# Performance work log

Hardware: AMD Instinct MI355X
Metric: run time of the kernel (lower is better)

The kernel has to match this reference:

```python
import jax, jax.numpy as jnp
import numpy as np

B, T, C, L = 128, 1024, 128, 128
EPS = 1e-7        # keras.backend.epsilon()
NEG = -1e30       # log-space -inf surrogate


def setup_inputs() -> dict:
    key = jax.random.key(0)
    k1, k2, k3, k4 = jax.random.split(key, 4)
    logits = jax.random.normal(k1, (B, T, C), dtype=jnp.float32)
    y_pred = jax.nn.softmax(logits, axis=-1)                      # ctc_batch_cost expects probs
    y_true = jax.random.randint(k2, (B, L), 0, C - 1)             # blank = C-1 excluded from labels
    input_len = jax.random.randint(k3, (B, 1), T // 2, T + 1)
    label_len = jax.random.randint(k4, (B, 1), L // 2, L + 1)
    return {"y_true": y_true, "y_pred": y_pred, "input_len": input_len, "label_len": label_len}


def _ctc_loss(y_pred, y_true, input_len, label_len):
    # Faithful port of keras ctc_batch_cost: blank index = C-1, merge repeated,
    # log(y_pred + eps), returns per-sample loss with shape [B, 1].
    log_probs = jnp.log(y_pred + EPS)                             # [B,T,C]
    b, t_max, c = log_probs.shape
    blank = c - 1
    l = y_true.shape[1]
    s = 2 * l + 1
    # extended label sequence: blank, l1, blank, l2, ..., blank   [B,S]
    ext = jnp.full((b, s), blank, dtype=y_true.dtype).at[:, 1::2].set(y_true)
    # emission log-prob of each extended symbol at each frame     [B,T,S]
    lp_ext = jnp.take_along_axis(
        log_probs, jnp.broadcast_to(ext[:, None, :], (b, t_max, s)), axis=2)
    # skip transition s-2 -> s allowed iff ext[s] != blank and ext[s] != ext[s-2]
    allow_skip = jnp.concatenate(
        [jnp.zeros((b, 2), bool), (ext[:, 2:] != blank) & (ext[:, 2:] != ext[:, :-2])], axis=1)
    alpha0 = jnp.full((b, s), NEG, dtype=log_probs.dtype).at[:, 0].set(0.0)
    in_len = input_len.reshape(b, 1).astype(jnp.int32)

    def step(alpha, xt):
        lp_t, t = xt                                              # lp_t: [B,S]
        a1 = jnp.pad(alpha[:, :-1], ((0, 0), (1, 0)), constant_values=NEG)
        a2 = jnp.where(allow_skip,
                       jnp.pad(alpha[:, :-2], ((0, 0), (2, 0)), constant_values=NEG), NEG)
        new = lp_t + jnp.logaddexp(jnp.logaddexp(alpha, a1), a2)
        new = jnp.where(t < in_len, new, alpha)                   # freeze past input_len
        return new, None

    alpha, _ = jax.lax.scan(step, alpha0, (jnp.swapaxes(lp_ext, 0, 1), jnp.arange(t_max)))
    lab = label_len.reshape(b, 1).astype(jnp.int32)
    a_last = jnp.take_along_axis(alpha, 2 * lab, axis=1)          # ends at final blank
    a_prev = jnp.take_along_axis(alpha, jnp.maximum(2 * lab - 1, 0), axis=1)  # or final label
    return -jnp.logaddexp(a_last, a_prev)                         # [B,1]


def reference(y_true, y_pred, input_len, label_len):
    return _ctc_loss(y_pred, y_true, input_len, label_len)
```

## Files before the change

kernel.cpp:

```cpp
#include <hip/hip_runtime.h>
#include <cstdint>

#define NB 128
#define NT 1024
#define NC 128
#define NL 128
#define NS 257
#define EPSF 1e-7f
#define LN2F 0.69314718055994530942f
#define NEGL2 -1.442695e30f

typedef float __attribute__((ext_vector_type(2))) v2f;

__device__ __forceinline__ float fexp2(float x){ return __builtin_amdgcn_exp2f(x); }
__device__ __forceinline__ float flog2(float x){ return __builtin_amdgcn_logf(x); }

__device__ __forceinline__ float shup1(float x){
    int r = __builtin_amdgcn_update_dpp(0, __float_as_int(x), 0x138, 0xf, 0xf, true);
    return __int_as_float(r);
}
__device__ __forceinline__ int shup1i(int x){
    return __builtin_amdgcn_update_dpp(0, x, 0x138, 0xf, 0xf, true);
}

__device__ __forceinline__ void dma16(const float* g, float* lds){
    __builtin_amdgcn_global_load_lds((const __attribute__((address_space(1))) void*)g,
                                     (__attribute__((address_space(3))) void*)lds,
                                     16, 0, 0);
}

#define VM_DRAIN() asm volatile("s_waitcnt vmcnt(0)" ::: "memory")

#define AS3U(p) ((unsigned)(size_t)(__attribute__((address_space(3))) void*)(p))

#define WAITLGKM(N) do{ asm volatile("s_waitcnt lgkmcnt(" #N ")" ::: "memory"); \
                        __builtin_amdgcn_sched_barrier(0); }while(0)

#define FILLA(S, O0,O1,O2,O3) do{ \
  asm volatile("ds_read2st64_b32 %0, %1 offset0:" #O0 " offset1:" #O1 : "=v"(S##B2[0]) : "v"(aB)); \
  asm volatile("ds_read2st64_b32 %0, %1 offset0:" #O2 " offset1:" #O3 : "=v"(S##B2[1]) : "v"(aB)); \
  asm volatile("ds_read2st64_b32 %0, %1 offset0:" #O0 " offset1:" #O1 : "=v"(S##A2[0]) : "v"(aA)); \
  asm volatile("ds_read2st64_b32 %0, %1 offset0:" #O2 " offset1:" #O3 : "=v"(S##A2[1]) : "v"(aA)); \
  asm volatile("ds_read2st64_b32 %0, %1 offset0:" #O0 " offset1:" #O1 : "=v"(S##C2[0]) : "v"(aC)); \
  asm volatile("ds_read2st64_b32 %0, %1 offset0:" #O2 " offset1:" #O3 : "=v"(S##C2[1]) : "v"(aC)); \
}while(0)

#define GROUP(S, gg) do{ \
    const v2f pb0 = S##B2[0] + E2, pa0 = S##A2[0] + E2, pc0 = S##C2[0] + E2; \
    const v2f pb1 = S##B2[1] + E2, pa1 = S##A2[1] + E2, pc1 = S##C2[1] + E2; \
    { const bool c_ = !freeze || ((k*32 + (gg)*4 + 0) < Tn); step1(pb0.x, pa0.x, pc0.x, c_); } \
    shm3 = shup1(m3); \
    { const bool c_ = !freeze || ((k*32 + (gg)*4 + 1) < Tn); step1(pb0.y, pa0.y, pc0.y, c_); } \
    shm3 = shup1(m3); \
    { const bool c_ = !freeze || ((k*32 + (gg)*4 + 2) < Tn); step1(pb1.x, pa1.x, pc1.x, c_); } \
    shm3 = shup1(m3); \
    { const bool c_ = !freeze || ((k*32 + (gg)*4 + 3) < Tn); step1(pb1.y, pa1.y, pc1.y, c_); } \
    boundary(early); }while(0)

__global__ __launch_bounds__(64,1)
void ctc_fwd_kernel(const int* __restrict__ y_true,
                    const float* __restrict__ y_pred,
                    const int* __restrict__ input_len,
                    const int* __restrict__ label_len,
                    float* __restrict__ out)
{
    __shared__ float buf[2][32 * NC];
    __shared__ float lg_alpha[NS + 3];

    const int b    = blockIdx.x;
    const int lane = threadIdx.x;
    const float* __restrict__ base = y_pred + (size_t)b * NT * NC;

    int Tn = input_len[b];
    Tn = Tn < 0 ? 0 : (Tn > NT ? NT : Tn);

    const int* __restrict__ yrow = y_true + b * NL;
    const int y0v = yrow[2 * lane]     & (NC - 1);
    const int y1v = yrow[2 * lane + 1] & (NC - 1);
    const int yp  = shup1i(y1v);
    const bool skip1 = (lane > 0) && (y0v != yp);
    const bool skip3 = (y1v != y0v);
    const bool isl0  = (lane == 0);
    const bool isl63 = (lane == 63);
    const float skip3f = skip3 ? 1.f : 0.f;

    const v2f E2 = { EPSF, EPSF };

    float m0 = isl0 ? 1.f : 0.f, m1 = 0.f, m2 = 0.f, m3 = 0.f, m4 = 0.f;
    int   ei  = 0;
    float f0  = isl0 ? 0.f : 1.f;
    float fs1 = skip1 ? f0 : 0.f;
    float shm3 = 0.f;

    v2f s0B2[2], s0A2[2], s0C2[2];
    v2f s1B2[2], s1A2[2], s1C2[2];
    v2f s2B2[2], s2A2[2], s2C2[2];

    auto dma_chunk = [&](int c){
        const float* gsrc = base + (size_t)c * 32 * NC;
        float* dst = &buf[c & 1][0];
        #pragma unroll
        for (int i = 0; i < 16; ++i)
            dma16(gsrc + i * 256 + lane * 4, dst + i * 256);
    };

    auto step1 = [&](float Pb, float Pa, float Pc, bool commit){
        float a1  = m3 + m2;
        float a2  = m2 + m1;
        float s43 = m4 + m3;
        float a5  = m1 + m0;
        float a6  = fmaf(m1,   skip3f, a1);
        float a7  = fmaf(shm3, fs1,    a5);
        float a4  = fmaf(shm3, f0,     m0);
        float n3 = Pc * a6;
        float n2 = Pb * a2;
        float n4 = Pb * s43;
        float n0 = Pb * a4;
        float n1 = Pa * a7;
        if (commit) { m0 = n0; m1 = n1; m2 = n2; m3 = n3; m4 = n4; }
    };

    auto boundary = [&](bool early){
        float mx = fmaxf(fmaxf(m0, m1), fmaxf(m2, m3));
        if (isl63) mx = fmaxf(mx, m4);
        const uint32_t bx = __float_as_uint(mx);
        const int eb = (int)(bx >> 23);
        const float inv = __uint_as_float((uint32_t)(254 - eb) << 23);
        const int de = eb - 127;
        int s_nb;
        if (early) {
            const bool dead = (mx == 0.f);
            int e1 = dead ? ei : (ei + de);
            int s1 = shup1i(e1);
            int e2 = (dead && !isl0) ? s1 : e1;
            int s2 = shup1i(e2);
            ei = (dead && !isl0) ? s2 : e2;
            s_nb = s2;
        } else {
            ei += de;
            s_nb = shup1i(ei);
        }
        int d = s_nb - ei;
        d = d < -126 ? -126 : (d > 126 ? 126 : d);
        f0 = isl0 ? 0.f : __uint_as_float((uint32_t)(d + 127) << 23);
        fs1 = skip1 ? f0 : 0.f;
        m0 *= inv; m1 *= inv; m2 *= inv; m3 *= inv; m4 *= inv;
        shm3 = shup1(m3);
    };

    auto chunkbody = [&](int k, bool early, bool freeze){
        const int h = k & 1;
        const unsigned aB = AS3U(&buf[h][NC - 1]);
        const unsigned aA = AS3U(&buf[h][y0v]);
        const unsigned aC = AS3U(&buf[h][y1v]);

        FILLA(s0,  0, 2, 4, 6);
        if (k + 1 < 32) dma_chunk(k + 1);
        FILLA(s1,  8,10,12,14);

        FILLA(s2, 16,18,20,22); WAITLGKM(12); GROUP(s0, 0);
        FILLA(s0, 24,26,28,30); WAITLGKM(12); GROUP(s1, 1);
        FILLA(s1, 32,34,36,38); WAITLGKM(12); GROUP(s2, 2);
        FILLA(s2, 40,42,44,46); WAITLGKM(12); GROUP(s0, 3);
        FILLA(s0, 48,50,52,54); WAITLGKM(12); GROUP(s1, 4);
        FILLA(s1, 56,58,60,62); WAITLGKM(12); GROUP(s2, 5);
                                WAITLGKM(6);  GROUP(s0, 6);
                                WAITLGKM(0);  GROUP(s1, 7);

        VM_DRAIN();
    };

    dma_chunk(0);
    VM_DRAIN();

    const int nfull = Tn >> 5;
    #pragma unroll 1
    for (int k = 0; k < 8; ++k)       chunkbody(k, true,  false);
    #pragma unroll 1
    for (int k = 8; k < nfull; ++k)   chunkbody(k, false, false);
    if (nfull < 32 && (Tn & 31))      chunkbody(nfull, false, true);

    const float e = (float)ei;
    lg_alpha[4 * lane + 0] = (m0 > 0.f) ? (e + flog2(m0)) : NEGL2;
    lg_alpha[4 * lane + 1] = (m1 > 0.f) ? (e + flog2(m1)) : NEGL2;
    lg_alpha[4 * lane + 2] = (m2 > 0.f) ? (e + flog2(m2)) : NEGL2;
    lg_alpha[4 * lane + 3] = (m3 > 0.f) ? (e + flog2(m3)) : NEGL2;
    if (isl63) lg_alpha[256] = (m4 > 0.f) ? (e + flog2(m4)) : NEGL2;
    __syncthreads();

    if (lane == 0) {
        int lab = label_len[b];
        lab = lab < 0 ? 0 : (lab > NL ? NL : lab);
        const int i_last = 2 * lab;
        const int i_prev = i_last > 0 ? i_last - 1 : 0;
        float A  = lg_alpha[i_last];
        float Bv = lg_alpha[i_prev];
        float mx = fmaxf(A, Bv);
        float r;
        if (mx < -1.0e29f) {
            r = mx;
        } else {
            float s = fexp2(A - mx) + fexp2(Bv - mx);
            r = mx + flog2(s);
        }
        out[b] = -r * LN2F;
    }
}

extern "C" void kernel_launch(void* const* d_in, const int* in_sizes, int n_in,
                              void* d_out, int out_size, void* d_ws, size_t ws_size,
                              hipStream_t stream) {
    const int*   y_true    = (const int*)d_in[0];
    const float* y_pred    = (const float*)d_in[1];
    const int*   input_len = (const int*)d_in[2];
    const int*   label_len = (const int*)d_in[3];
    float* outp = (float*)d_out;
    ctc_fwd_kernel<<<dim3(NB), dim3(64), 0, stream>>>(y_true, y_pred, input_len, label_len, outp);
}
```

Before: 133.3 us.

## Add producer wave to prefetch chunks and pre-add epsilon into LDS image

Splits the block into a producer wave and a consumer wave. The producer DMAs chunks of y_pred into raw LDS buffers, adds epsilon with vector LDS ops and writes an image buffer, synchronising with s_barrier. The consumer runs the alpha recursion directly on the eps-adjusted image without DMA issue or vmcnt drains in its critical path, and the lane-0 f0 special-casing is dropped. This adds barrier overhead per chunk, doubles LDS usage, and the producer's early return with barriers still pending may be a hazard.

```diff
diff --git a/kernel.cpp b/kernel.cpp
--- a/kernel.cpp
+++ b/kernel.cpp
@@ -11,6 +11,7 @@
 #define NEGL2 -1.442695e30f
 
 typedef float __attribute__((ext_vector_type(2))) v2f;
+typedef float __attribute__((ext_vector_type(4))) v4f;
 
 __device__ __forceinline__ float fexp2(float x){ return __builtin_amdgcn_exp2f(x); }
 __device__ __forceinline__ float flog2(float x){ return __builtin_amdgcn_logf(x); }
@@ -35,6 +36,9 @@
 
 #define WAITLGKM(N) do{ asm volatile("s_waitcnt lgkmcnt(" #N ")" ::: "memory"); \
                         __builtin_amdgcn_sched_barrier(0); }while(0)
+
+#define BAR_C() asm volatile("s_barrier" ::: "memory")
+#define BAR_P() asm volatile("s_waitcnt lgkmcnt(0)\n\ts_barrier" ::: "memory")
 
 #define FILLA(S, O0,O1,O2,O3) do{ \
   asm volatile("ds_read2st64_b32 %0, %1 offset0:" #O0 " offset1:" #O1 : "=v"(S##B2[0]) : "v"(aB)); \
@@ -46,33 +50,65 @@
 }while(0)
 
 #define GROUP(S, gg) do{ \
-    const v2f pb0 = S##B2[0] + E2, pa0 = S##A2[0] + E2, pc0 = S##C2[0] + E2; \
-    const v2f pb1 = S##B2[1] + E2, pa1 = S##A2[1] + E2, pc1 = S##C2[1] + E2; \
-    { const bool c_ = !freeze || ((k*32 + (gg)*4 + 0) < Tn); step1(pb0.x, pa0.x, pc0.x, c_); } \
+    { const bool c_ = !freeze || ((k*32 + (gg)*4 + 0) < Tn); step1(S##B2[0].x, S##A2[0].x, S##C2[0].x, c_); } \
     shm3 = shup1(m3); \
-    { const bool c_ = !freeze || ((k*32 + (gg)*4 + 1) < Tn); step1(pb0.y, pa0.y, pc0.y, c_); } \
+    { const bool c_ = !freeze || ((k*32 + (gg)*4 + 1) < Tn); step1(S##B2[0].y, S##A2[0].y, S##C2[0].y, c_); } \
     shm3 = shup1(m3); \
-    { const bool c_ = !freeze || ((k*32 + (gg)*4 + 2) < Tn); step1(pb1.x, pa1.x, pc1.x, c_); } \
+    { const bool c_ = !freeze || ((k*32 + (gg)*4 + 2) < Tn); step1(S##B2[1].x, S##A2[1].x, S##C2[1].x, c_); } \
     shm3 = shup1(m3); \
-    { const bool c_ = !freeze || ((k*32 + (gg)*4 + 3) < Tn); step1(pb1.y, pa1.y, pc1.y, c_); } \
+    { const bool c_ = !freeze || ((k*32 + (gg)*4 + 3) < Tn); step1(S##B2[1].y, S##A2[1].y, S##C2[1].y, c_); } \
     boundary(early); }while(0)
 
-__global__ __launch_bounds__(64,1)
+__global__ __launch_bounds__(128,1)
 void ctc_fwd_kernel(const int* __restrict__ y_true,
                     const float* __restrict__ y_pred,
                     const int* __restrict__ input_len,
                     const int* __restrict__ label_len,
                     float* __restrict__ out)
 {
-    __shared__ float buf[2][32 * NC];
+    __shared__ __align__(16) float raw[2][32 * NC];
+    __shared__ __align__(16) float img[2][32 * NC];
     __shared__ float lg_alpha[NS + 3];
 
     const int b    = blockIdx.x;
-    const int lane = threadIdx.x;
-    const float* __restrict__ base = y_pred + (size_t)b * NT * NC;
+    const int tid  = threadIdx.x;
+    const int lane = tid & 63;
 
     int Tn = input_len[b];
     Tn = Tn < 0 ? 0 : (Tn > NT ? NT : Tn);
+    const int nfull   = Tn >> 5;
+    const int partial = (nfull < 32 && (Tn & 31)) ? 1 : 0;
+    const int CT      = nfull + partial;
+
+    if (tid >= 64) {
+        const float* __restrict__ base = y_pred + (size_t)b * NT * NC;
+        auto dma_chunk = [&](int c){
+            const float* gsrc = base + (size_t)c * 32 * NC;
+            float* dst = &raw[c & 1][0];
+            #pragma unroll
+            for (int i = 0; i < 16; ++i)
+                dma16(gsrc + i * 256 + lane * 4, dst + i * 256);
+        };
+        auto eps_pass = [&](int c){
+            const v4f* s = (const v4f*)&raw[c & 1][0];
+            v4f*       d = (v4f*)&img[c & 1][0];
+            #pragma unroll
+            for (int j = 0; j < 16; ++j){
+                v4f v = s[j * 64 + lane];
+                v += (v4f){EPSF, EPSF, EPSF, EPSF};
+                d[j * 64 + lane] = v;
+            }
+        };
+        dma_chunk(0); VM_DRAIN(); eps_pass(0);
+        dma_chunk(1);
+        #pragma unroll 1
+        for (int k = 0; k < CT; ++k){
+            BAR_P();
+            if (k + 1 < CT){ VM_DRAIN(); eps_pass(k + 1); }
+            if (k + 2 < CT) dma_chunk(k + 2);
+        }
+        return;
+    }
 
     const int* __restrict__ yrow = y_true + b * NL;
     const int y0v = yrow[2 * lane]     & (NC - 1);
@@ -84,25 +120,15 @@
     const bool isl63 = (lane == 63);
     const float skip3f = skip3 ? 1.f : 0.f;
 
-    const v2f E2 = { EPSF, EPSF };
-
     float m0 = isl0 ? 1.f : 0.f, m1 = 0.f, m2 = 0.f, m3 = 0.f, m4 = 0.f;
     int   ei  = 0;
-    float f0  = isl0 ? 0.f : 1.f;
-    float fs1 = skip1 ? f0 : 0.f;
+    float f0  = 1.f;
+    float fs1 = skip1 ? 1.f : 0.f;
     float shm3 = 0.f;
 
     v2f s0B2[2], s0A2[2], s0C2[2];
     v2f s1B2[2], s1A2[2], s1C2[2];
     v2f s2B2[2], s2A2[2], s2C2[2];
-
-    auto dma_chunk = [&](int c){
-        const float* gsrc = base + (size_t)c * 32 * NC;
-        float* dst = &buf[c & 1][0];
-        #pragma unroll
-        for (int i = 0; i < 16; ++i)
-            dma16(gsrc + i * 256 + lane * 4, dst + i * 256);
-    };
 
     auto step1 = [&](float Pb, float Pa, float Pc, bool commit){
         float a1  = m3 + m2;
@@ -142,7 +168,7 @@
         }
         int d = s_nb - ei;
         d = d < -126 ? -126 : (d > 126 ? 126 : d);
-        f0 = isl0 ? 0.f : __uint_as_float((uint32_t)(d + 127) << 23);
+        f0 = __uint_as_float((uint32_t)(d + 127) << 23);
         fs1 = skip1 ? f0 : 0.f;
         m0 *= inv; m1 *= inv; m2 *= inv; m3 *= inv; m4 *= inv;
         shm3 = shup1(m3);
@@ -150,12 +176,11 @@
 
     auto chunkbody = [&](int k, bool early, bool freeze){
         const int h = k & 1;
-        const unsigned aB = AS3U(&buf[h][NC - 1]);
-        const unsigned aA = AS3U(&buf[h][y0v]);
-        const unsigned aC = AS3U(&buf[h][y1v]);
+        const unsigned aB = AS3U(&img[h][NC - 1]);
+        const unsigned aA = AS3U(&img[h][y0v]);
+        const unsigned aC = AS3U(&img[h][y1v]);
 
         FILLA(s0,  0, 2, 4, 6);
-        if (k + 1 < 32) dma_chunk(k + 1);
         FILLA(s1,  8,10,12,14);
 
         FILLA(s2, 16,18,20,22); WAITLGKM(12); GROUP(s0, 0);
@@ -166,19 +191,13 @@
         FILLA(s1, 56,58,60,62); WAITLGKM(12); GROUP(s2, 5);
                                 WAITLGKM(6);  GROUP(s0, 6);
                                 WAITLGKM(0);  GROUP(s1, 7);
-
-        VM_DRAIN();
     };
 
-    dma_chunk(0);
-    VM_DRAIN();
-
-    const int nfull = Tn >> 5;
     #pragma unroll 1
-    for (int k = 0; k < 8; ++k)       chunkbody(k, true,  false);
+    for (int k = 0; k < 8; ++k)      { BAR_C(); chunkbody(k, true,  false); }
     #pragma unroll 1
-    for (int k = 8; k < nfull; ++k)   chunkbody(k, false, false);
-    if (nfull < 32 && (Tn & 31))      chunkbody(nfull, false, true);
+    for (int k = 8; k < nfull; ++k)  { BAR_C(); chunkbody(k, false, false); }
+    if (partial)                     { BAR_C(); chunkbody(nfull, false, true); }
 
     const float e = (float)ei;
     lg_alpha[4 * lane + 0] = (m0 > 0.f) ? (e + flog2(m0)) : NEGL2;
@@ -186,7 +205,7 @@
     lg_alpha[4 * lane + 2] = (m2 > 0.f) ? (e + flog2(m2)) : NEGL2;
     lg_alpha[4 * lane + 3] = (m3 > 0.f) ? (e + flog2(m3)) : NEGL2;
     if (isl63) lg_alpha[256] = (m4 > 0.f) ? (e + flog2(m4)) : NEGL2;
-    __syncthreads();
+    asm volatile("s_waitcnt lgkmcnt(0)" ::: "memory");
 
     if (lane == 0) {
         int lab = label_len[b];
@@ -215,5 +234,5 @@
     const int*   input_len = (const int*)d_in[2];
     const int*   label_len = (const int*)d_in[3];
     float* outp = (float*)d_out;
-    ctc_fwd_kernel<<<dim3(NB), dim3(64), 0, stream>>>(y_true, y_pred, input_len, label_len, outp);
-}
+    ctc_fwd_kernel<<<dim3(NB), dim3(128), 0, stream>>>(y_true, y_pred, input_len, label_len, outp);
+}
```

Result: faster. 129.0 us (-3.3%).
